# Performance work log

Hardware: AMD Instinct MI355X
Metric: run time of the kernel (lower is better)

Reference implementation:

```python
import jax, jax.numpy as jnp
import numpy as np

B, C_IN, C_OUT = 4, 8, 8
P_IN, P_OUT = 16384, 4096
N_EVAL = 1_000_000
SPATIAL = 2
HID = 64
DECAY = (P_IN / 16) ** 2  # 1048576.0; bump support: ||z||^4 <= 1/DECAY -> ||z|| <= 1/32


def setup_inputs() -> dict:
    key = jax.random.key(0)
    ks = jax.random.split(key, 8)
    features = jax.random.normal(ks[0], (B, C_IN, P_IN), jnp.float32)
    # offsets inside the bump support (max ||z|| ~ 0.0283 < 0.03125 keeps 1 - DECAY*||z||^4 > 0)
    eval_locs = (jax.random.uniform(ks[1], (N_EVAL, SPATIAL), jnp.float32) * 2.0 - 1.0) * 0.02
    quad_weights = jax.random.uniform(ks[2], (P_IN,), jnp.float32, 0.5, 1.5) / P_IN
    # filter MLP: spatial_dim -> 64 -> 64 -> C_IN*C_OUT, Sin activations, no bias
    W0 = jax.random.normal(ks[3], (SPATIAL, HID), jnp.float32) / np.float32(np.sqrt(SPATIAL))
    W1 = jax.random.normal(ks[4], (HID, HID), jnp.float32) / np.float32(np.sqrt(HID))
    W2 = jax.random.normal(ks[5], (HID, C_IN * C_OUT), jnp.float32) / np.float32(np.sqrt(HID))
    eval_idx_out = jnp.sort(jax.random.randint(ks[6], (N_EVAL,), 0, P_OUT, jnp.int32))
    eval_idx_in = jax.random.randint(ks[7], (N_EVAL,), 0, P_IN, jnp.int32)
    return dict(features=features, eval_locs=eval_locs, quad_weights=quad_weights,
                W0=W0, W1=W1, W2=W2, eval_idx_out=eval_idx_out, eval_idx_in=eval_idx_in)


def reference(features, eval_locs, quad_weights, W0, W1, W2, eval_idx_out, eval_idx_in):
    # per-eval-point filter G(z): (N, C_in, C_out)
    h = jnp.sin(eval_locs @ W0)
    h = jnp.sin(h @ W1)
    filt = (h @ W2).reshape(-1, C_IN, C_OUT)
    # bump(z) = exp(1 - 1/(1 - decay*||z||^4))
    r4 = jnp.sum(eval_locs * eval_locs, axis=-1) ** 2          # (N,)
    bump = jnp.exp(1.0 - 1.0 / (1.0 - DECAY * r4))             # (N,)
    w = bump * quad_weights[eval_idx_in]                       # (N,)
    gathered = features[:, :, eval_idx_in]                     # (B, C_in, N)
    # fused bump/quad weighting + per-point matmul
    values = jnp.einsum('n,bin,nij->nbj', w, gathered, filt)   # (N, B, C_out)
    # scatter-reduce sum over output-point index
    integral = jax.ops.segment_sum(values, eval_idx_out, num_segments=P_OUT)  # (P_out, B, C_out)
    return jnp.transpose(integral, (1, 2, 0))                  # (B, C_out, P_out)
```

## Files before the change

### kernel.cpp

```cpp
#include <hip/hip_runtime.h>

#define NEV    1000000
#define POUT   4096
#define PIN    16384
#define INV2PI 0.15915494309189535f

typedef __bf16 bf16x8 __attribute__((ext_vector_type(8)));
typedef float  f32x16 __attribute__((ext_vector_type(16)));

#define FT_FLOATS (32 * PIN)

#define LH_ST 36
#define LW_ST 36

#define SEL_HI 0x07060302u
#define SEL_LO 0x05040100u

__device__ __forceinline__ unsigned pack_hl(float v) {
    const unsigned b = __builtin_bit_cast(unsigned, v);
    const float hb = __builtin_bit_cast(float, b & 0xFFFF0000u);
    const float lo = v - hb;
    return __builtin_amdgcn_perm(b, __builtin_bit_cast(unsigned, lo), SEL_HI);
}

#define GEMM3(accv, ahi_, alo_, bhi_, blo_)                                          \
    accv = __builtin_amdgcn_mfma_f32_32x32x16_bf16(ahi_, bhi_, accv, 0, 0, 0);       \
    accv = __builtin_amdgcn_mfma_f32_32x32x16_bf16(ahi_, blo_, accv, 0, 0, 0);       \
    accv = __builtin_amdgcn_mfma_f32_32x32x16_bf16(alo_, bhi_, accv, 0, 0, 0);

__global__ __launch_bounds__(256) void prep_k(const float* __restrict__ f,
                                              float* __restrict__ ws) {
    __shared__ float tile[32][33];
    const int t = threadIdx.x;
    const int p0 = blockIdx.x * 32;
    #pragma unroll
    for (int rep = 0; rep < 4; ++rep) {
        const int idx = rep * 256 + t;
        const int c = idx >> 5, pl = idx & 31;
        tile[pl][c] = f[c * PIN + p0 + pl];
    }
    __syncthreads();
    #pragma unroll
    for (int rep = 0; rep < 4; ++rep) {
        const int idx = rep * 256 + t;
        const int pl = idx >> 5, c = idx & 31;
        ws[(p0 + pl) * 32 + c] = tile[pl][c];
    }
}

template <int MODE>
__global__ __launch_bounds__(64, 2) void quadconv_mfma_k(
    const float* __restrict__ features,
    const float* __restrict__ eval_locs,
    const float* __restrict__ quad_weights,
    const float* __restrict__ W0,
    const float* __restrict__ W1,
    const float* __restrict__ W2,
    const int* __restrict__ eio,
    const int* __restrict__ eii,
    const float* __restrict__ ws,
    float* __restrict__ out)
{
    __shared__ unsigned lh[64 * LH_ST];
    __shared__ unsigned lw[32 * LW_ST];
    const int lane = threadIdx.x;
    const int n    = lane & 31;
    const int hl   = lane >> 5;
    const int p    = blockIdx.x;

    int start, end;
    {
        const int tgt = p + (lane & 1);
        int lo = 0, hi = NEV;
        while (lo < hi) { int m = (lo + hi) >> 1; if (eio[m] < tgt) lo = m + 1; else hi = m; }
        start = __shfl(lo, 0);
        end   = __shfl(lo, 1);
    }

    bf16x8 a1hi[2][4], a1lo[2][4];
    #pragma unroll
    for (int mb = 0; mb < 2; ++mb) {
        #pragma unroll
        for (int t = 0; t < 4; ++t) {
            unsigned hw[4], lw_[4];
            #pragma unroll
            for (int i = 0; i < 4; ++i) {
                const float v0 = W1[(8 * hl + 2 * i + 16 * t) * 64 + n + 32 * mb] * INV2PI;
                const float v1 = W1[(8 * hl + 2 * i + 1 + 16 * t) * 64 + n + 32 * mb] * INV2PI;
                const unsigned b0 = __builtin_bit_cast(unsigned, v0);
                const unsigned b1 = __builtin_bit_cast(unsigned, v1);
                const float l0 = v0 - __builtin_bit_cast(float, b0 & 0xFFFF0000u);
                const float l1 = v1 - __builtin_bit_cast(float, b1 & 0xFFFF0000u);
                hw[i]  = __builtin_amdgcn_perm(b1, b0, SEL_HI);
                lw_[i] = __builtin_amdgcn_perm(__builtin_bit_cast(unsigned, l1),
                                               __builtin_bit_cast(unsigned, l0), SEL_HI);
            }
            a1hi[mb][t] = __builtin_bit_cast(bf16x8, make_uint4(hw[0], hw[1], hw[2], hw[3]));
            a1lo[mb][t] = __builtin_bit_cast(bf16x8, make_uint4(lw_[0], lw_[1], lw_[2], lw_[3]));
        }
    }

    f32x16 T[2];
    #pragma unroll
    for (int mb = 0; mb < 2; ++mb)
        #pragma unroll
        for (int r = 0; r < 16; ++r) T[mb][r] = 0.f;

    unsigned* Lhw = &lh[4 * hl * LH_ST + n];
    unsigned* Lww = &lw[16 * hl * LW_ST + n];
    const unsigned* Lhr = &lh[n * LH_ST + 8 * hl];
    const unsigned* Lwr = &lw[n * LW_ST + 8 * hl];

    const int nt = (end - start + 31) >> 5;

    for (int tile = 0; tile < nt; ++tile) {
        const int e  = start + tile * 32 + n;
        const bool valid = (e < end);
        const int ec = valid ? e : (end - 1);
        const float2 x = ((const float2*)eval_locs)[ec];
        const int ii = eii[ec];

        const float r2 = x.x * x.x + x.y * x.y;
        const float dd = 1.0f - 1048576.0f * r2 * r2;
        float wgt = __expf(1.0f - 1.0f / dd) * quad_weights[ii];
        if (!valid) wgt = 0.f;

        const float xs = x.x * INV2PI;
        const float ys = x.y * INV2PI;

        f32x16 acc1[2];
        #pragma unroll
        for (int mb = 0; mb < 2; ++mb)
            #pragma unroll
            for (int r = 0; r < 16; ++r) acc1[mb][r] = 0.f;

        #pragma unroll
        for (int t = 0; t < 4; ++t) {
            const int k0 = 16 * t + 8 * hl;
            float s[8];
            #pragma unroll
            for (int q = 0; q < 8; ++q)
                s[q] = __builtin_amdgcn_sinf(fmaf(xs, W0[k0 + q], ys * W0[64 + k0 + q]));
            unsigned hw[4], lw_[4];
            #pragma unroll
            for (int i = 0; i < 4; ++i) {
                const unsigned b0 = __builtin_bit_cast(unsigned, s[2 * i]);
                const unsigned b1 = __builtin_bit_cast(unsigned, s[2 * i + 1]);
                const float l0 = s[2 * i]     - __builtin_bit_cast(float, b0 & 0xFFFF0000u);
                const float l1 = s[2 * i + 1] - __builtin_bit_cast(float, b1 & 0xFFFF0000u);
                hw[i]  = __builtin_amdgcn_perm(b1, b0, SEL_HI);
                lw_[i] = __builtin_amdgcn_perm(__builtin_bit_cast(unsigned, l1),
                                               __builtin_bit_cast(unsigned, l0), SEL_HI);
            }
            const bf16x8 bhi = __builtin_bit_cast(bf16x8, make_uint4(hw[0], hw[1], hw[2], hw[3]));
            const bf16x8 blo = __builtin_bit_cast(bf16x8, make_uint4(lw_[0], lw_[1], lw_[2], lw_[3]));
            GEMM3(acc1[0], a1hi[0][t], a1lo[0][t], bhi, blo);
            GEMM3(acc1[1], a1hi[1][t], a1lo[1][t], bhi, blo);
        }

        #pragma unroll
        for (int mb = 0; mb < 2; ++mb) {
            #pragma unroll
            for (int r = 0; r < 16; ++r) {
                const int row = ((r & 3) + 8 * (r >> 2) + 32 * mb);
                Lhw[row * LH_ST] = pack_hl(__builtin_amdgcn_sinf(acc1[mb][r]));
            }
        }

        {
            float g[16];
            if constexpr (MODE == 0) {
                const float4* gp = (const float4*)(ws + ii * 32 + 16 * hl);
                const float4 G0 = gp[0], G1 = gp[1], G2 = gp[2], G3 = gp[3];
                g[0]=G0.x; g[1]=G0.y; g[2]=G0.z; g[3]=G0.w;
                g[4]=G1.x; g[5]=G1.y; g[6]=G1.z; g[7]=G1.w;
                g[8]=G2.x; g[9]=G2.y; g[10]=G2.z; g[11]=G2.w;
                g[12]=G3.x; g[13]=G3.y; g[14]=G3.z; g[15]=G3.w;
            } else {
                #pragma unroll
                for (int v = 0; v < 16; ++v) g[v] = features[(16 * hl + v) * PIN + ii];
            }
            #pragma unroll
            for (int v = 0; v < 16; ++v) Lww[v * LW_ST] = pack_hl(wgt * g[v]);
        }

        #pragma unroll
        for (int kt = 0; kt < 2; ++kt) {
            const uint4 p0 = *(const uint4*)(Lwr + 16 * kt);
            const uint4 p1 = *(const uint4*)(Lwr + 16 * kt + 4);
            const bf16x8 bh = __builtin_bit_cast(bf16x8, make_uint4(
                __builtin_amdgcn_perm(p0.y, p0.x, SEL_HI),
                __builtin_amdgcn_perm(p0.w, p0.z, SEL_HI),
                __builtin_amdgcn_perm(p1.y, p1.x, SEL_HI),
                __builtin_amdgcn_perm(p1.w, p1.z, SEL_HI)));
            const bf16x8 bl = __builtin_bit_cast(bf16x8, make_uint4(
                __builtin_amdgcn_perm(p0.y, p0.x, SEL_LO),
                __builtin_amdgcn_perm(p0.w, p0.z, SEL_LO),
                __builtin_amdgcn_perm(p1.y, p1.x, SEL_LO),
                __builtin_amdgcn_perm(p1.w, p1.z, SEL_LO)));
            #pragma unroll
            for (int mb = 0; mb < 2; ++mb) {
                const uint4 q0 = *(const uint4*)(Lhr + 32 * mb * LH_ST + 16 * kt);
                const uint4 q1 = *(const uint4*)(Lhr + 32 * mb * LH_ST + 16 * kt + 4);
                const bf16x8 ah = __builtin_bit_cast(bf16x8, make_uint4(
                    __builtin_amdgcn_perm(q0.y, q0.x, SEL_HI),
                    __builtin_amdgcn_perm(q0.w, q0.z, SEL_HI),
                    __builtin_amdgcn_perm(q1.y, q1.x, SEL_HI),
                    __builtin_amdgcn_perm(q1.w, q1.z, SEL_HI)));
                const bf16x8 al = __builtin_bit_cast(bf16x8, make_uint4(
                    __builtin_amdgcn_perm(q0.y, q0.x, SEL_LO),
                    __builtin_amdgcn_perm(q0.w, q0.z, SEL_LO),
                    __builtin_amdgcn_perm(q1.y, q1.x, SEL_LO),
                    __builtin_amdgcn_perm(q1.w, q1.z, SEL_LO)));
                GEMM3(T[mb], ah, al, bh, bl);
            }
        }
    }

    {
        const int i = n & 7, b = n >> 3;
        float pj[8];
        #pragma unroll
        for (int j = 0; j < 8; ++j) pj[j] = 0.f;
        #pragma unroll
        for (int mb = 0; mb < 2; ++mb) {
            #pragma unroll
            for (int r = 0; r < 16; ++r) {
                const int khid = (r & 3) + 8 * (r >> 2) + 4 * hl + 32 * mb;
                const float tv = T[mb][r];
                const float4 w20 = *(const float4*)(W2 + khid * 64 + i * 8);
                const float4 w21 = *(const float4*)(W2 + khid * 64 + i * 8 + 4);
                pj[0] = fmaf(tv, w20.x, pj[0]);
                pj[1] = fmaf(tv, w20.y, pj[1]);
                pj[2] = fmaf(tv, w20.z, pj[2]);
                pj[3] = fmaf(tv, w20.w, pj[3]);
                pj[4] = fmaf(tv, w21.x, pj[4]);
                pj[5] = fmaf(tv, w21.y, pj[5]);
                pj[6] = fmaf(tv, w21.z, pj[6]);
                pj[7] = fmaf(tv, w21.w, pj[7]);
            }
        }
        #pragma unroll
        for (int j = 0; j < 8; ++j) {
            float v = pj[j];
            v += __shfl_xor(v, 1);
            v += __shfl_xor(v, 2);
            v += __shfl_xor(v, 4);
            v += __shfl_xor(v, 32);
            pj[j] = v;
        }
        if (i == 0 && hl == 0) {
            #pragma unroll
            for (int j = 0; j < 8; ++j) out[b * (8 * POUT) + j * POUT + p] = pj[j];
        }
    }
}

extern "C" void kernel_launch(void* const* d_in, const int* in_sizes, int n_in,
                              void* d_out, int out_size, void* d_ws, size_t ws_size,
                              hipStream_t stream) {
    const float* features  = (const float*)d_in[0];
    const float* eval_locs = (const float*)d_in[1];
    const float* qw        = (const float*)d_in[2];
    const float* W0        = (const float*)d_in[3];
    const float* W1        = (const float*)d_in[4];
    const float* W2        = (const float*)d_in[5];
    const int*   eio       = (const int*)d_in[6];
    const int*   eii       = (const int*)d_in[7];
    float* out = (float*)d_out;
    float* ws  = (float*)d_ws;

    if (ws_size >= (size_t)FT_FLOATS * 4) {
        prep_k<<<PIN / 32, 256, 0, stream>>>(features, ws);
        quadconv_mfma_k<0><<<POUT, 64, 0, stream>>>(features, eval_locs, qw, W0, W1, W2,
                                                    eio, eii, ws, out);
    } else {
        quadconv_mfma_k<2><<<POUT, 64, 0, stream>>>(features, eval_locs, qw, W0, W1, W2,
                                                    eio, eii, ws, out);
    }
}
```

Before: 152.9 us.

## Transpose layer-1 GEMM to keep hidden activations in registers via permlane32 swap

The first-layer MFMA now has its operands swapped, so each lane's accumulator rows already match the A-operand layout of the second GEMM. The hidden activations are repacked in registers with v_permlane32_swap instead of a round trip through the lh shared-memory buffer. Separately, the per-output segment boundaries are computed once by extra blocks in the prep kernel and stored in the workspace, which removes each block's own binary search over eio. This cuts LDS traffic and the serial search latency, at the cost of more live registers and a larger prep launch.

```diff
diff --git a/kernel.cpp b/kernel.cpp
--- a/kernel.cpp
+++ b/kernel.cpp
@@ -8,9 +8,10 @@
 typedef __bf16 bf16x8 __attribute__((ext_vector_type(8)));
 typedef float  f32x16 __attribute__((ext_vector_type(16)));
 
+#define SEG_OFF   0
+#define FT_OFF    4160
 #define FT_FLOATS (32 * PIN)
 
-#define LH_ST 36
 #define LW_ST 36
 
 #define SEL_HI 0x07060302u
@@ -28,23 +29,35 @@
     accv = __builtin_amdgcn_mfma_f32_32x32x16_bf16(ahi_, blo_, accv, 0, 0, 0);       \
     accv = __builtin_amdgcn_mfma_f32_32x32x16_bf16(alo_, bhi_, accv, 0, 0, 0);
 
+#define PLSWAP(a_, b_) asm("v_permlane32_swap_b32 %0, %1" : "+v"(a_), "+v"(b_))
+
 __global__ __launch_bounds__(256) void prep_k(const float* __restrict__ f,
+                                              const int* __restrict__ eio,
                                               float* __restrict__ ws) {
-    __shared__ float tile[32][33];
-    const int t = threadIdx.x;
-    const int p0 = blockIdx.x * 32;
-    #pragma unroll
-    for (int rep = 0; rep < 4; ++rep) {
-        const int idx = rep * 256 + t;
-        const int c = idx >> 5, pl = idx & 31;
-        tile[pl][c] = f[c * PIN + p0 + pl];
-    }
-    __syncthreads();
-    #pragma unroll
-    for (int rep = 0; rep < 4; ++rep) {
-        const int idx = rep * 256 + t;
-        const int pl = idx >> 5, c = idx & 31;
-        ws[(p0 + pl) * 32 + c] = tile[pl][c];
+    const int bid = blockIdx.x, t = threadIdx.x;
+    if (bid < 512) {
+        __shared__ float tile[32][33];
+        const int p0 = bid * 32;
+        #pragma unroll
+        for (int rep = 0; rep < 4; ++rep) {
+            const int idx = rep * 256 + t;
+            const int c = idx >> 5, pl = idx & 31;
+            tile[pl][c] = f[c * PIN + p0 + pl];
+        }
+        __syncthreads();
+        #pragma unroll
+        for (int rep = 0; rep < 4; ++rep) {
+            const int idx = rep * 256 + t;
+            const int pl = idx >> 5, c = idx & 31;
+            ws[FT_OFF + (p0 + pl) * 32 + c] = tile[pl][c];
+        }
+    } else {
+        int* seg = (int*)ws + SEG_OFF;
+        const int q = (bid - 512) * 256 + t;
+        int lo = 0, hi = NEV;
+        while (lo < hi) { int m = (lo + hi) >> 1; if (eio[m] < q) lo = m + 1; else hi = m; }
+        seg[q] = lo;
+        if (q == 0) seg[POUT] = NEV;
     }
 }
 
@@ -61,7 +74,6 @@
     const float* __restrict__ ws,
     float* __restrict__ out)
 {
-    __shared__ unsigned lh[64 * LH_ST];
     __shared__ unsigned lw[32 * LW_ST];
     const int lane = threadIdx.x;
     const int n    = lane & 31;
@@ -69,7 +81,10 @@
     const int p    = blockIdx.x;
 
     int start, end;
-    {
+    if constexpr (MODE == 0) {
+        const int* seg = (const int*)ws + SEG_OFF;
+        start = seg[p]; end = seg[p + 1];
+    } else {
         const int tgt = p + (lane & 1);
         int lo = 0, hi = NEV;
         while (lo < hi) { int m = (lo + hi) >> 1; if (eio[m] < tgt) lo = m + 1; else hi = m; }
@@ -77,16 +92,16 @@
         end   = __shfl(lo, 1);
     }
 
-    bf16x8 a1hi[2][4], a1lo[2][4];
+    bf16x8 b1hi[2][4], b1lo[2][4];
     #pragma unroll
-    for (int mb = 0; mb < 2; ++mb) {
+    for (int cb = 0; cb < 2; ++cb) {
         #pragma unroll
         for (int t = 0; t < 4; ++t) {
             unsigned hw[4], lw_[4];
             #pragma unroll
             for (int i = 0; i < 4; ++i) {
-                const float v0 = W1[(8 * hl + 2 * i + 16 * t) * 64 + n + 32 * mb] * INV2PI;
-                const float v1 = W1[(8 * hl + 2 * i + 1 + 16 * t) * 64 + n + 32 * mb] * INV2PI;
+                const float v0 = W1[(8 * hl + 2 * i + 16 * t) * 64 + n + 32 * cb] * INV2PI;
+                const float v1 = W1[(8 * hl + 2 * i + 1 + 16 * t) * 64 + n + 32 * cb] * INV2PI;
                 const unsigned b0 = __builtin_bit_cast(unsigned, v0);
                 const unsigned b1 = __builtin_bit_cast(unsigned, v1);
                 const float l0 = v0 - __builtin_bit_cast(float, b0 & 0xFFFF0000u);
@@ -95,8 +110,8 @@
                 lw_[i] = __builtin_amdgcn_perm(__builtin_bit_cast(unsigned, l1),
                                                __builtin_bit_cast(unsigned, l0), SEL_HI);
             }
-            a1hi[mb][t] = __builtin_bit_cast(bf16x8, make_uint4(hw[0], hw[1], hw[2], hw[3]));
-            a1lo[mb][t] = __builtin_bit_cast(bf16x8, make_uint4(lw_[0], lw_[1], lw_[2], lw_[3]));
+            b1hi[cb][t] = __builtin_bit_cast(bf16x8, make_uint4(hw[0], hw[1], hw[2], hw[3]));
+            b1lo[cb][t] = __builtin_bit_cast(bf16x8, make_uint4(lw_[0], lw_[1], lw_[2], lw_[3]));
         }
     }
 
@@ -106,9 +121,7 @@
         #pragma unroll
         for (int r = 0; r < 16; ++r) T[mb][r] = 0.f;
 
-    unsigned* Lhw = &lh[4 * hl * LH_ST + n];
     unsigned* Lww = &lw[16 * hl * LW_ST + n];
-    const unsigned* Lhr = &lh[n * LH_ST + 8 * hl];
     const unsigned* Lwr = &lw[n * LW_ST + 8 * hl];
 
     const int nt = (end - start + 31) >> 5;
@@ -130,9 +143,9 @@
 
         f32x16 acc1[2];
         #pragma unroll
-        for (int mb = 0; mb < 2; ++mb)
-            #pragma unroll
-            for (int r = 0; r < 16; ++r) acc1[mb][r] = 0.f;
+        for (int cb = 0; cb < 2; ++cb)
+            #pragma unroll
+            for (int r = 0; r < 16; ++r) acc1[cb][r] = 0.f;
 
         #pragma unroll
         for (int t = 0; t < 4; ++t) {
@@ -152,25 +165,22 @@
                 lw_[i] = __builtin_amdgcn_perm(__builtin_bit_cast(unsigned, l1),
                                                __builtin_bit_cast(unsigned, l0), SEL_HI);
             }
-            const bf16x8 bhi = __builtin_bit_cast(bf16x8, make_uint4(hw[0], hw[1], hw[2], hw[3]));
-            const bf16x8 blo = __builtin_bit_cast(bf16x8, make_uint4(lw_[0], lw_[1], lw_[2], lw_[3]));
-            GEMM3(acc1[0], a1hi[0][t], a1lo[0][t], bhi, blo);
-            GEMM3(acc1[1], a1hi[1][t], a1lo[1][t], bhi, blo);
-        }
-
-        #pragma unroll
-        for (int mb = 0; mb < 2; ++mb) {
-            #pragma unroll
-            for (int r = 0; r < 16; ++r) {
-                const int row = ((r & 3) + 8 * (r >> 2) + 32 * mb);
-                Lhw[row * LH_ST] = pack_hl(__builtin_amdgcn_sinf(acc1[mb][r]));
-            }
-        }
+            const bf16x8 ahi = __builtin_bit_cast(bf16x8, make_uint4(hw[0], hw[1], hw[2], hw[3]));
+            const bf16x8 alo = __builtin_bit_cast(bf16x8, make_uint4(lw_[0], lw_[1], lw_[2], lw_[3]));
+            GEMM3(acc1[0], ahi, alo, b1hi[0][t], b1lo[0][t]);
+            GEMM3(acc1[1], ahi, alo, b1hi[1][t], b1lo[1][t]);
+        }
+
+        unsigned Q0[16], Q1[16];
+        #pragma unroll
+        for (int r = 0; r < 16; ++r) Q0[r] = pack_hl(__builtin_amdgcn_sinf(acc1[0][r]));
+        #pragma unroll
+        for (int r = 0; r < 16; ++r) Q1[r] = pack_hl(__builtin_amdgcn_sinf(acc1[1][r]));
 
         {
             float g[16];
             if constexpr (MODE == 0) {
-                const float4* gp = (const float4*)(ws + ii * 32 + 16 * hl);
+                const float4* gp = (const float4*)(ws + FT_OFF + ii * 32 + 16 * hl);
                 const float4 G0 = gp[0], G1 = gp[1], G2 = gp[2], G3 = gp[3];
                 g[0]=G0.x; g[1]=G0.y; g[2]=G0.z; g[3]=G0.w;
                 g[4]=G1.x; g[5]=G1.y; g[6]=G1.z; g[7]=G1.w;
@@ -182,6 +192,14 @@
             }
             #pragma unroll
             for (int v = 0; v < 16; ++v) Lww[v * LW_ST] = pack_hl(wgt * g[v]);
+        }
+
+        #pragma unroll
+        for (int kt = 0; kt < 2; ++kt) {
+            #pragma unroll
+            for (int j = 0; j < 4; ++j) { PLSWAP(Q0[8 * kt + j], Q0[8 * kt + 4 + j]); }
+            #pragma unroll
+            for (int j = 0; j < 4; ++j) { PLSWAP(Q1[8 * kt + j], Q1[8 * kt + 4 + j]); }
         }
 
         #pragma unroll
@@ -198,21 +216,31 @@
                 __builtin_amdgcn_perm(p0.w, p0.z, SEL_LO),
                 __builtin_amdgcn_perm(p1.y, p1.x, SEL_LO),
                 __builtin_amdgcn_perm(p1.w, p1.z, SEL_LO)));
-            #pragma unroll
-            for (int mb = 0; mb < 2; ++mb) {
-                const uint4 q0 = *(const uint4*)(Lhr + 32 * mb * LH_ST + 16 * kt);
-                const uint4 q1 = *(const uint4*)(Lhr + 32 * mb * LH_ST + 16 * kt + 4);
+            {
                 const bf16x8 ah = __builtin_bit_cast(bf16x8, make_uint4(
-                    __builtin_amdgcn_perm(q0.y, q0.x, SEL_HI),
-                    __builtin_amdgcn_perm(q0.w, q0.z, SEL_HI),
-                    __builtin_amdgcn_perm(q1.y, q1.x, SEL_HI),
-                    __builtin_amdgcn_perm(q1.w, q1.z, SEL_HI)));
+                    __builtin_amdgcn_perm(Q0[8*kt+1], Q0[8*kt+0], SEL_HI),
+                    __builtin_amdgcn_perm(Q0[8*kt+3], Q0[8*kt+2], SEL_HI),
+                    __builtin_amdgcn_perm(Q0[8*kt+5], Q0[8*kt+4], SEL_HI),
+                    __builtin_amdgcn_perm(Q0[8*kt+7], Q0[8*kt+6], SEL_HI)));
                 const bf16x8 al = __builtin_bit_cast(bf16x8, make_uint4(
-                    __builtin_amdgcn_perm(q0.y, q0.x, SEL_LO),
-                    __builtin_amdgcn_perm(q0.w, q0.z, SEL_LO),
-                    __builtin_amdgcn_perm(q1.y, q1.x, SEL_LO),
-                    __builtin_amdgcn_perm(q1.w, q1.z, SEL_LO)));
-                GEMM3(T[mb], ah, al, bh, bl);
+                    __builtin_amdgcn_perm(Q0[8*kt+1], Q0[8*kt+0], SEL_LO),
+                    __builtin_amdgcn_perm(Q0[8*kt+3], Q0[8*kt+2], SEL_LO),
+                    __builtin_amdgcn_perm(Q0[8*kt+5], Q0[8*kt+4], SEL_LO),
+                    __builtin_amdgcn_perm(Q0[8*kt+7], Q0[8*kt+6], SEL_LO)));
+                GEMM3(T[0], ah, al, bh, bl);
+            }
+            {
+                const bf16x8 ah = __builtin_bit_cast(bf16x8, make_uint4(
+                    __builtin_amdgcn_perm(Q1[8*kt+1], Q1[8*kt+0], SEL_HI),
+                    __builtin_amdgcn_perm(Q1[8*kt+3], Q1[8*kt+2], SEL_HI),
+                    __builtin_amdgcn_perm(Q1[8*kt+5], Q1[8*kt+4], SEL_HI),
+                    __builtin_amdgcn_perm(Q1[8*kt+7], Q1[8*kt+6], SEL_HI)));
+                const bf16x8 al = __builtin_bit_cast(bf16x8, make_uint4(
+                    __builtin_amdgcn_perm(Q1[8*kt+1], Q1[8*kt+0], SEL_LO),
+                    __builtin_amdgcn_perm(Q1[8*kt+3], Q1[8*kt+2], SEL_LO),
+                    __builtin_amdgcn_perm(Q1[8*kt+5], Q1[8*kt+4], SEL_LO),
+                    __builtin_amdgcn_perm(Q1[8*kt+7], Q1[8*kt+6], SEL_LO)));
+                GEMM3(T[1], ah, al, bh, bl);
             }
         }
     }
@@ -270,8 +298,8 @@
     float* out = (float*)d_out;
     float* ws  = (float*)d_ws;
 
-    if (ws_size >= (size_t)FT_FLOATS * 4) {
-        prep_k<<<PIN / 32, 256, 0, stream>>>(features, ws);
+    if (ws_size >= (size_t)(FT_OFF + FT_FLOATS) * 4) {
+        prep_k<<<512 + POUT / 256, 256, 0, stream>>>(features, eio, ws);
         quadconv_mfma_k<0><<<POUT, 64, 0, stream>>>(features, eval_locs, qw, W0, W1, W2,
                                                     eio, eii, ws, out);
     } else {
```

New measurement: 136.3 us. 1.12x faster.
